# Kernel tuning notes

Measured on AMD Instinct MI355X. Metric: run time of the kernel, lower is better.

The kernel has to match this reference:

```python
import jax, jax.numpy as jnp
import numpy as np

HIDDEN = 512
HEADS = 8
HEAD_DIM = HIDDEN // HEADS
EPS_LN = 1e-5
EPS_ATTN = 1e-6


def setup_inputs() -> dict:
    key = jax.random.key(0)
    ks = jax.random.split(key, 12)
    B, S, N, D = 4, 12, 2048, HIDDEN
    s = 1.0 / np.sqrt(D)
    x = jax.random.normal(ks[0], (B, S, N, D), dtype=jnp.float32)
    Wq = jax.random.normal(ks[1], (D, D), dtype=jnp.float32) * s
    bq = jnp.zeros((D,), dtype=jnp.float32)
    Wk = jax.random.normal(ks[2], (D, D), dtype=jnp.float32) * s
    bk = jnp.zeros((D,), dtype=jnp.float32)
    Wv = jax.random.normal(ks[3], (D, D), dtype=jnp.float32) * s
    bv = jnp.zeros((D,), dtype=jnp.float32)
    Wo = jax.random.normal(ks[4], (D, D), dtype=jnp.float32) * s
    bo = jnp.zeros((D,), dtype=jnp.float32)
    ln_g = jnp.ones((D,), dtype=jnp.float32)
    ln_b = jnp.zeros((D,), dtype=jnp.float32)
    return {"x": x, "Wq": Wq, "bq": bq, "Wk": Wk, "bk": bk,
            "Wv": Wv, "bv": bv, "Wo": Wo, "bo": bo,
            "ln_g": ln_g, "ln_b": ln_b}


def _layer_norm(x, g, b):
    mu = jnp.mean(x, axis=-1, keepdims=True)
    var = jnp.var(x, axis=-1, keepdims=True)
    return (x - mu) * jax.lax.rsqrt(var + EPS_LN) * g + b


def reference(x, Wq, bq, Wk, bk, Wv, bv, Wo, bo, ln_g, ln_b):
    B, S, N, D = x.shape
    L = S * N  # flattened spatiotemporal tokens
    residual = x
    h = _layer_norm(x, ln_g, ln_b).reshape(B, L, D)
    # projections; [B, L, D] -> [B, H, L, hd]
    def split_heads(t):
        return t.reshape(B, L, HEADS, HEAD_DIM).transpose(0, 2, 1, 3)
    q = split_heads(h @ Wq.T + bq)
    k = split_heads(h @ Wk.T + bk)
    v = split_heads(h @ Wv.T + bv)
    # elu+1 feature map
    q = jax.nn.elu(q) + 1.0
    k = jax.nn.elu(k) + 1.0
    # kv outer product: [B, H, hd, hd]
    kv = jnp.einsum('bhld,bhle->bhde', k, v)
    out = jnp.einsum('bhld,bhde->bhle', q, kv)
    normalizer = jnp.einsum('bhld,bhd->bhl', q, k.sum(axis=2))
    out = out / (normalizer[..., None] + EPS_ATTN)
    out = out.transpose(0, 2, 1, 3).reshape(B, L, D)
    out = out @ Wo.T + bo
    out = out.reshape(B, S, N, D)
    return out + residual
```

## Files before the change

### kernel.cpp

```cpp
#include <hip/hip_runtime.h>
#include <hip/hip_bf16.h>
#include <stdint.h>

#define DDIM 512
#define NHEAD 8
#define BATCH 4
#define LTOK 24576
#define MROWS 98304
#define QKV_MBLK 384
#define KVCH 96
#define PTILE 4160

typedef __attribute__((ext_vector_type(8))) short short8;
typedef __attribute__((ext_vector_type(4))) float f32x4;

__device__ __forceinline__ float bf2f(unsigned short u) {
  union { unsigned int i; float f; } c; c.i = ((unsigned int)u) << 16; return c.f;
}
__device__ __forceinline__ unsigned short f2bf(float f) {
  __hip_bfloat16 h = __float2bfloat16(f);
  return __builtin_bit_cast(unsigned short, h);
}
__device__ __forceinline__ void gload16(const void* g, void* l) {
  __builtin_amdgcn_global_load_lds((const __attribute__((address_space(1))) void*)g,
                                   (__attribute__((address_space(3))) void*)l, 16, 0, 0);
}
__device__ __forceinline__ float elu1(float v) { return (v > 0.f) ? (v + 1.f) : __expf(v); }

__global__ __launch_bounds__(256) void wprep(const float* __restrict__ Wq, const float* __restrict__ bq,
                                             const float* __restrict__ Wk, const float* __restrict__ bk,
                                             const float* __restrict__ Wv, const float* __restrict__ bv,
                                             const float* __restrict__ Wo,
                                             unsigned short* __restrict__ wf,
                                             unsigned short* __restrict__ wob,
                                             float* __restrict__ biasf) {
  long t = (long)blockIdx.x * 256 + threadIdx.x;
  if (t < 786432) {
    int f = (int)(t >> 9), c = (int)(t & 511);
    const float* src;
    if (f < 1024) { int hh = f >> 7, kv = (f >> 6) & 1, d = f & 63;
                    src = (kv ? Wv : Wk) + (long)(hh * 64 + d) * 512; }
    else          src = Wq + (long)(f - 1024) * 512;
    wf[t] = f2bf(src[c]);
  } else if (t < 786432 + 262144) {
    long i = t - 786432; wob[i] = f2bf(Wo[i]);
  } else if (t < 786432 + 262144 + 1536) {
    int f = (int)(t - (786432 + 262144));
    float v;
    if (f < 1024) { int hh = f >> 7, kv = (f >> 6) & 1, d = f & 63; v = (kv ? bv : bk)[hh * 64 + d]; }
    else v = bq[f - 1024];
    biasf[f] = v;
  }
}

__global__ __launch_bounds__(256) void ln_kernel(const float* __restrict__ x,
                                                 const float* __restrict__ g,
                                                 const float* __restrict__ b,
                                                 unsigned short* __restrict__ h) {
  int wv = threadIdx.x >> 6, lane = threadIdx.x & 63;
  long row = (long)blockIdx.x * 4 + wv;
  const float* xr = x + row * DDIM + lane * 8;
  float4 v0 = *(const float4*)xr;
  float4 v1 = *(const float4*)(xr + 4);
  float s  = v0.x + v0.y + v0.z + v0.w + v1.x + v1.y + v1.z + v1.w;
  float s2 = v0.x*v0.x + v0.y*v0.y + v0.z*v0.z + v0.w*v0.w
           + v1.x*v1.x + v1.y*v1.y + v1.z*v1.z + v1.w*v1.w;
  #pragma unroll
  for (int o = 32; o; o >>= 1) { s += __shfl_xor(s, o); s2 += __shfl_xor(s2, o); }
  float mu = s * (1.0f / DDIM);
  float var = s2 * (1.0f / DDIM) - mu * mu;
  float rs = rsqrtf(var + 1e-5f);
  float4 g0 = *(const float4*)(g + lane * 8);
  float4 g1 = *(const float4*)(g + lane * 8 + 4);
  float4 b0 = *(const float4*)(b + lane * 8);
  float4 b1 = *(const float4*)(b + lane * 8 + 4);
  short8 o;
  o[0] = (short)f2bf((v0.x - mu) * rs * g0.x + b0.x);
  o[1] = (short)f2bf((v0.y - mu) * rs * g0.y + b0.y);
  o[2] = (short)f2bf((v0.z - mu) * rs * g0.z + b0.z);
  o[3] = (short)f2bf((v0.w - mu) * rs * g0.w + b0.w);
  o[4] = (short)f2bf((v1.x - mu) * rs * g1.x + b1.x);
  o[5] = (short)f2bf((v1.y - mu) * rs * g1.y + b1.y);
  o[6] = (short)f2bf((v1.z - mu) * rs * g1.z + b1.z);
  o[7] = (short)f2bf((v1.w - mu) * rs * g1.w + b1.w);
  *(short8*)(h + row * DDIM + lane * 8) = o;
}

__device__ __forceinline__ short8 ldsfrag(const unsigned short* h, int row, int kg) {
  return *(const short8*)&h[row * 32 + ((kg ^ ((row >> 1) & 3)) << 3)];
}

__device__ __forceinline__ void stage_half(const unsigned short* gbase,
                                           unsigned short* ldsbase, int tid) {
  #pragma unroll
  for (int i = 0; i < 2; i++) {
    int c = i * 512 + tid;
    int rr = c >> 2, cc = c & 3;
    int sc = ((cc ^ ((rr >> 1) & 3)) << 3);
    gload16(gbase + (long)rr * DDIM + sc, ldsbase + c * 8);
  }
}

template <int VMP1, int VMP3, bool S01, bool S23>
__device__ __forceinline__ void ktile(int t, unsigned short* lds,
                                      const unsigned short* Ab, const unsigned short* Wb,
                                      f32x4 (&acc)[8][4],
                                      int wm, int wn, int lr, int kg, int tid) {
  const int buf = t & 1;
  unsigned short* A0l = lds + (buf * 2 + 0) * 8192;
  unsigned short* A1l = lds + (buf * 2 + 1) * 8192;
  unsigned short* B0l = lds + 32768 + (buf * 2 + 0) * 8192;
  unsigned short* B1l = lds + 32768 + (buf * 2 + 1) * 8192;
  unsigned short* A1n = lds + ((buf ^ 1) * 2 + 1) * 8192;
  unsigned short* B1n = lds + 32768 + ((buf ^ 1) * 2 + 1) * 8192;
  short8 a[4], b[4];

  #pragma unroll
  for (int m = 0; m < 4; m++) a[m] = ldsfrag(A0l, wm * 128 + m * 16 + lr, kg);
  #pragma unroll
  for (int n = 0; n < 4; n++) b[n] = ldsfrag(B0l, wn * 64 + n * 16 + lr, kg);
  if (S01) stage_half(Ab + (long)(t + 1) * 64 + 32, A1n, tid);
  __builtin_amdgcn_s_barrier();
  __builtin_amdgcn_s_setprio(1);
  #pragma unroll
  for (int m = 0; m < 4; m++)
    #pragma unroll
    for (int n = 0; n < 4; n++)
      acc[m][n] = __builtin_amdgcn_mfma_f32_16x16x32_bf16(a[m], b[n], acc[m][n], 0, 0, 0);
  __builtin_amdgcn_s_setprio(0);
  __builtin_amdgcn_s_barrier();
  __builtin_amdgcn_sched_barrier(0);

  #pragma unroll
  for (int m = 0; m < 4; m++) a[m] = ldsfrag(A0l, wm * 128 + (4 + m) * 16 + lr, kg);
  if (S01) stage_half(Wb + (long)(t + 1) * 64 + 32, B1n, tid);
  __builtin_amdgcn_s_barrier();
  __builtin_amdgcn_s_setprio(1);
  #pragma unroll
  for (int m = 0; m < 4; m++)
    #pragma unroll
    for (int n = 0; n < 4; n++)
      acc[4 + m][n] = __builtin_amdgcn_mfma_f32_16x16x32_bf16(a[m], b[n], acc[4 + m][n], 0, 0, 0);
  __builtin_amdgcn_s_setprio(0);
  asm volatile("s_waitcnt vmcnt(%0)" :: "i"(VMP1) : "memory");
  __builtin_amdgcn_s_barrier();
  __builtin_amdgcn_sched_barrier(0);

  #pragma unroll
  for (int m = 0; m < 4; m++) a[m] = ldsfrag(A1l, wm * 128 + m * 16 + lr, kg);
  #pragma unroll
  for (int n = 0; n < 4; n++) b[n] = ldsfrag(B1l, wn * 64 + n * 16 + lr, kg);
  if (S23) stage_half(Ab + (long)(t + 2) * 64, A0l, tid);
  __builtin_amdgcn_s_barrier();
  __builtin_amdgcn_s_setprio(1);
  #pragma unroll
  for (int m = 0; m < 4; m++)
    #pragma unroll
    for (int n = 0; n < 4; n++)
      acc[m][n] = __builtin_amdgcn_mfma_f32_16x16x32_bf16(a[m], b[n], acc[m][n], 0, 0, 0);
  __builtin_amdgcn_s_setprio(0);
  __builtin_amdgcn_s_barrier();
  __builtin_amdgcn_sched_barrier(0);

  #pragma unroll
  for (int m = 0; m < 4; m++) a[m] = ldsfrag(A1l, wm * 128 + (4 + m) * 16 + lr, kg);
  if (S23) stage_half(Wb + (long)(t + 2) * 64, B0l, tid);
  __builtin_amdgcn_s_barrier();
  __builtin_amdgcn_s_setprio(1);
  #pragma unroll
  for (int m = 0; m < 4; m++)
    #pragma unroll
    for (int n = 0; n < 4; n++)
      acc[4 + m][n] = __builtin_amdgcn_mfma_f32_16x16x32_bf16(a[m], b[n], acc[4 + m][n], 0, 0, 0);
  __builtin_amdgcn_s_setprio(0);
  asm volatile("s_waitcnt vmcnt(%0)" :: "i"(VMP3) : "memory");
  __builtin_amdgcn_s_barrier();
  __builtin_amdgcn_sched_barrier(0);
}

__device__ __forceinline__ void kloop256(unsigned short* lds,
                                         const unsigned short* Ab, const unsigned short* Wb,
                                         f32x4 (&acc)[8][4],
                                         int wm, int wn, int lr, int kg, int tid) {
  stage_half(Ab,       lds + 0 * 8192, tid);
  stage_half(Wb,       lds + 32768 + 0 * 8192, tid);
  stage_half(Ab + 32,  lds + 1 * 8192, tid);
  stage_half(Wb + 32,  lds + 32768 + 1 * 8192, tid);
  stage_half(Ab + 64,  lds + 2 * 8192, tid);
  stage_half(Wb + 64,  lds + 32768 + 2 * 8192, tid);
  asm volatile("s_waitcnt vmcnt(8)" ::: "memory");
  __builtin_amdgcn_s_barrier();
  __builtin_amdgcn_sched_barrier(0);

  #pragma unroll 1
  for (int i = 0; i < 3; i++) {
    ktile<8, 8, true, true>(2 * i,     lds, Ab, Wb, acc, wm, wn, lr, kg, tid);
    ktile<8, 8, true, true>(2 * i + 1, lds, Ab, Wb, acc, wm, wn, lr, kg, tid);
  }
  ktile<8, 4, true, false>(6, lds, Ab, Wb, acc, wm, wn, lr, kg, tid);
  ktile<0, 63, false, false>(7, lds, Ab, Wb, acc, wm, wn, lr, kg, tid);
}

__global__ __launch_bounds__(512, 2) void qkv_gemm(const unsigned short* __restrict__ A,
                                                   const unsigned short* __restrict__ wf,
                                                   const float* __restrict__ biasf,
                                                   unsigned short* __restrict__ qbuf,
                                                   unsigned short* __restrict__ part) {
  __shared__ unsigned short lds[65536];

  int tid = threadIdx.x;
  int wv = tid >> 6, lane = tid & 63;
  int wm = wv >> 2, wn = wv & 3;
  int kg = lane >> 4, lr = lane & 15;

  int lin = blockIdx.x;
  int g = lin / 48, r = lin % 48;
  int xb = g * 8 + (r & 7);
  int y  = r >> 3;
  long mBase = (long)xb * 256;
  int nBase = y * 256;

  const unsigned short* Ab = A + mBase * DDIM;
  const unsigned short* Wb = wf + (long)nBase * DDIM;

  f32x4 acc[8][4];
  #pragma unroll
  for (int m = 0; m < 8; m++)
    #pragma unroll
    for (int n = 0; n < 4; n++) acc[m][n] = (f32x4){0.f, 0.f, 0.f, 0.f};

  kloop256(lds, Ab, Wb, acc, wm, wn, lr, kg, tid);
  __syncthreads();

  if (y < 4) {
    unsigned short* kT = lds;
    unsigned short* vT = lds + 16896;
    int batch = xb / KVCH;
    int cIdx  = xb % KVCH;

    {
      int rr = 64 + (tid >> 5), cc = tid & 31;
      short8 z;
      #pragma unroll
      for (int j = 0; j < 8; j++) z[j] = (rr == 64) ? (short)0x3F80 : (short)0;
      *(short8*)&vT[rr * 264 + cc * 8] = z;
    }

    #pragma unroll 1
    for (int p = 0; p < 2; p++) {
      if ((wn >> 1) == p) {
        bool isV = wn & 1;
        #pragma unroll
        for (int n = 0; n < 4; n++) {
          int feat = n * 16 + lr;
          float bv = biasf[nBase + wn * 64 + n * 16 + lr];
          #pragma unroll
          for (int m = 0; m < 8; m++)
            #pragma unroll
            for (int j = 0; j < 4; j++) {
              int tok = wm * 128 + m * 16 + kg * 4 + j;
              float v = acc[m][n][j] + bv;
              if (!isV) kT[feat * 264 + tok] = f2bf(elu1(v));
              else      vT[feat * 264 + tok] = f2bf(v);
            }
        }
      }
      __syncthreads();

      int mt = wv & 3, ngrp = wv >> 2;
      int h = y * 2 + p;
      long pbase = ((long)(batch * 8 + h) * KVCH + cIdx) * PTILE;
      if (!ngrp) {
        f32x4 pa0 = {0,0,0,0}, pa1 = {0,0,0,0}, pa2 = {0,0,0,0};
        #pragma unroll
        for (int kk = 0; kk < 8; kk++) {
          short8 af = *(const short8*)&kT[(mt * 16 + lr) * 264 + kk * 32 + kg * 8];
          short8 b0 = *(const short8*)&vT[(0 * 16 + lr) * 264 + kk * 32 + kg * 8];
          short8 b1 = *(const short8*)&vT[(1 * 16 + lr) * 264 + kk * 32 + kg * 8];
          short8 b2 = *(const short8*)&vT[(2 * 16 + lr) * 264 + kk * 32 + kg * 8];
          pa0 = __builtin_amdgcn_mfma_f32_16x16x32_bf16(af, b0, pa0, 0, 0, 0);
          pa1 = __builtin_amdgcn_mfma_f32_16x16x32_bf16(af, b1, pa1, 0, 0, 0);
          pa2 = __builtin_amdgcn_mfma_f32_16x16x32_bf16(af, b2, pa2, 0, 0, 0);
        }
        #pragma unroll
        for (int j = 0; j < 4; j++) {
          int d = mt * 16 + kg * 4 + j;
          part[pbase + d * 64 + (0 * 16 + lr)] = f2bf(pa0[j]);
          part[pbase + d * 64 + (1 * 16 + lr)] = f2bf(pa1[j]);
          part[pbase + d * 64 + (2 * 16 + lr)] = f2bf(pa2[j]);
        }
      } else {
        f32x4 pa0 = {0,0,0,0}, pa1 = {0,0,0,0};
        #pragma unroll
        for (int kk = 0; kk < 8; kk++) {
          short8 af = *(const short8*)&kT[(mt * 16 + lr) * 264 + kk * 32 + kg * 8];
          short8 b0 = *(const short8*)&vT[(3 * 16 + lr) * 264 + kk * 32 + kg * 8];
          short8 b1 = *(const short8*)&vT[(4 * 16 + lr) * 264 + kk * 32 + kg * 8];
          pa0 = __builtin_amdgcn_mfma_f32_16x16x32_bf16(af, b0, pa0, 0, 0, 0);
          pa1 = __builtin_amdgcn_mfma_f32_16x16x32_bf16(af, b1, pa1, 0, 0, 0);
        }
        #pragma unroll
        for (int j = 0; j < 4; j++) {
          int d = mt * 16 + kg * 4 + j;
          part[pbase + d * 64 + (3 * 16 + lr)] = f2bf(pa0[j]);
          if (lr == 0) part[pbase + 4096 + d] = f2bf(pa1[j]);
        }
      }
      __syncthreads();
    }
  } else {
    unsigned short* Cs = lds;
    int qc0 = (y - 4) * 256;
    #pragma unroll 1
    for (int half = 0; half < 2; half++) {
      if (wm == half) {
        #pragma unroll
        for (int n = 0; n < 4; n++) {
          int col = wn * 64 + n * 16 + lr;
          float bv = biasf[nBase + col];
          #pragma unroll
          for (int m = 0; m < 8; m++)
            #pragma unroll
            for (int j = 0; j < 4; j++) {
              int rowl = m * 16 + kg * 4 + j;
              Cs[rowl * 264 + col] = f2bf(elu1(acc[m][n][j] + bv));
            }
        }
      }
      __syncthreads();
      #pragma unroll
      for (int i = 0; i < 8; i++) {
        int idx = i * 512 + tid;
        int row = idx >> 5, ch = idx & 31;
        *(short8*)&qbuf[(mBase + half * 128 + row) * DDIM + qc0 + ch * 8] =
            *(const short8*)&Cs[row * 264 + ch * 8];
      }
      __syncthreads();
    }
  }
}

__global__ __launch_bounds__(256) void kv_final(const unsigned short* __restrict__ part,
                                                unsigned short* __restrict__ kvD,
                                                float* __restrict__ ksum) {
  int bh = blockIdx.x;
  int gidx = blockIdx.y * 256 + threadIdx.x;
  if (gidx >= 520) return;
  long idx0 = (long)gidx * 8;
  const unsigned short* base = part + (long)bh * KVCH * PTILE + idx0;
  float s[8];
  #pragma unroll
  for (int j = 0; j < 8; j++) s[j] = 0.f;
  #pragma unroll 4
  for (int c = 0; c < KVCH; c++) {
    short8 v = *(const short8*)(base + (long)c * PTILE);
    #pragma unroll
    for (int j = 0; j < 8; j++) s[j] += bf2f((unsigned short)v[j]);
  }
  if (idx0 < 4096) {
    short8 o;
    #pragma unroll
    for (int j = 0; j < 8; j++) o[j] = (short)f2bf(s[j]);
    *(short8*)&kvD[bh * 4096 + idx0] = o;
  } else {
    int d0 = (int)(idx0 - 4096);
    #pragma unroll
    for (int j = 0; j < 8; j++) ksum[bh * 64 + d0 + j] = s[j];
  }
}

__global__ __launch_bounds__(512) void w2_gemm(const unsigned short* __restrict__ kvD,
                                               const unsigned short* __restrict__ wob,
                                               unsigned short* __restrict__ Bmat) {
  __shared__ unsigned short W2s[512 * 72];
  int t = threadIdx.x, wv = t >> 6, lane = t & 63;
  int kg = lane >> 4, lr = lane & 15;
  int bh = blockIdx.x, b = bh >> 3, h = bh & 7;
  const unsigned short* kva = kvD + bh * 4096;

  short8 a[4][2];
  #pragma unroll
  for (int m = 0; m < 4; m++)
    #pragma unroll
    for (int kk = 0; kk < 2; kk++)
      a[m][kk] = *(const short8*)&kva[(m * 16 + lr) * 64 + kk * 32 + kg * 8];

  f32x4 acc[4][4];
  #pragma unroll
  for (int m = 0; m < 4; m++)
    #pragma unroll
    for (int n = 0; n < 4; n++) acc[m][n] = (f32x4){0.f, 0.f, 0.f, 0.f};

  #pragma unroll
  for (int n = 0; n < 4; n++) {
    int c = wv * 64 + n * 16 + lr;
    #pragma unroll
    for (int kk = 0; kk < 2; kk++) {
      short8 bfr = *(const short8*)&wob[(long)c * 512 + h * 64 + kk * 32 + kg * 8];
      #pragma unroll
      for (int m = 0; m < 4; m++)
        acc[m][n] = __builtin_amdgcn_mfma_f32_16x16x32_bf16(a[m][kk], bfr, acc[m][n], 0, 0, 0);
    }
  }
  #pragma unroll
  for (int m = 0; m < 4; m++)
    #pragma unroll
    for (int n = 0; n < 4; n++)
      #pragma unroll
      for (int j = 0; j < 4; j++)
        W2s[(wv * 64 + n * 16 + lr) * 72 + m * 16 + kg * 4 + j] = f2bf(acc[m][n][j]);
  __syncthreads();
  #pragma unroll
  for (int pp = 0; pp < 8; pp++) {
    int idx = pp * 512 + t;
    int c = idx >> 3, ch = (idx & 7) * 8;
    *(short8*)&Bmat[(long)b * 262144 + (long)c * 512 + h * 64 + ch] =
        *(const short8*)&W2s[c * 72 + ch];
  }
}

__global__ __launch_bounds__(256) void qscale(unsigned short* __restrict__ q,
                                              const float* __restrict__ ksum) {
  int wv = threadIdx.x >> 6, lane = threadIdx.x & 63;
  long row = (long)blockIdx.x * 4 + wv;
  int batch = (int)(row / LTOK);
  int bh = batch * 8 + (lane >> 3);
  unsigned short* qr = q + row * DDIM + lane * 8;
  short8 qv = *(const short8*)qr;
  const float* ks = ksum + bh * 64 + (lane & 7) * 8;
  float4 k0 = *(const float4*)ks;
  float4 k1 = *(const float4*)(ks + 4);
  float qf[8];
  #pragma unroll
  for (int j = 0; j < 8; j++) qf[j] = bf2f((unsigned short)qv[j]);
  float n = qf[0]*k0.x + qf[1]*k0.y + qf[2]*k0.z + qf[3]*k0.w
          + qf[4]*k1.x + qf[5]*k1.y + qf[6]*k1.z + qf[7]*k1.w;
  n += __shfl_xor(n, 1);
  n += __shfl_xor(n, 2);
  n += __shfl_xor(n, 4);
  float s = 1.0f / (n + 1e-6f);
  short8 o;
  #pragma unroll
  for (int j = 0; j < 8; j++) o[j] = (short)f2bf(qf[j] * s);
  *(short8*)qr = o;
}

__global__ __launch_bounds__(512, 2) void ogemm(const unsigned short* __restrict__ A,
                                                const unsigned short* __restrict__ Bm,
                                                const float* __restrict__ bo,
                                                const float* __restrict__ xres,
                                                float* __restrict__ out) {
  __shared__ unsigned short lds[65536];

  int tid = threadIdx.x;
  int wv = tid >> 6, lane = tid & 63;
  int wm = wv >> 2, wn = wv & 3;
  int kg = lane >> 4, lr = lane & 15;

  int lin = blockIdx.x;
  int g = lin >> 4, r = lin & 15;
  int xb = g * 8 + (r & 7);
  int y  = r >> 3;
  long mBase = (long)xb * 256;
  int nBase = y * 256;
  int batch = xb / 96;

  const unsigned short* Ab = A + mBase * DDIM;
  const unsigned short* Wb = Bm + (long)batch * 262144 + (long)nBase * DDIM;

  f32x4 acc[8][4];
  #pragma unroll
  for (int m = 0; m < 8; m++)
    #pragma unroll
    for (int n = 0; n < 4; n++) acc[m][n] = (f32x4){0.f, 0.f, 0.f, 0.f};

  kloop256(lds, Ab, Wb, acc, wm, wn, lr, kg, tid);
  __syncthreads();

  float* Cs = (float*)lds;
  #pragma unroll 1
  for (int half = 0; half < 2; half++) {
    if (wm == half) {
      #pragma unroll
      for (int n = 0; n < 4; n++) {
        int col = wn * 64 + n * 16 + lr;
        float bv = bo[nBase + col];
        #pragma unroll
        for (int m = 0; m < 8; m++)
          #pragma unroll
          for (int j = 0; j < 4; j++) {
            int lrow = m * 16 + kg * 4 + j;
            Cs[lrow * 256 + (col ^ (((lrow >> 2) & 3) << 4))] = acc[m][n][j] + bv;
          }
      }
    }
    __syncthreads();
    #pragma unroll
    for (int it = 0; it < 16; it++) {
      int idx = it * 512 + tid;
      int row = idx >> 6, c4 = idx & 63;
      int pcol = (c4 * 4) ^ (((row >> 2) & 3) << 4);
      long goff = (mBase + half * 128 + row) * DDIM + nBase + c4 * 4;
      float4 rv = *(const float4*)&xres[goff];
      float4 cv = *(const float4*)&Cs[row * 256 + pcol];
      float4 ov; ov.x = cv.x + rv.x; ov.y = cv.y + rv.y; ov.z = cv.z + rv.z; ov.w = cv.w + rv.w;
      *(float4*)&out[goff] = ov;
    }
    __syncthreads();
  }
}

extern "C" void kernel_launch(void* const* d_in, const int* in_sizes, int n_in,
                              void* d_out, int out_size, void* d_ws, size_t ws_size,
                              hipStream_t stream) {
  const float* x    = (const float*)d_in[0];
  const float* Wq   = (const float*)d_in[1];
  const float* bq   = (const float*)d_in[2];
  const float* Wk   = (const float*)d_in[3];
  const float* bk   = (const float*)d_in[4];
  const float* Wv   = (const float*)d_in[5];
  const float* bv   = (const float*)d_in[6];
  const float* Wo   = (const float*)d_in[7];
  const float* bo   = (const float*)d_in[8];
  const float* ln_g = (const float*)d_in[9];
  const float* ln_b = (const float*)d_in[10];

  char* ws = (char*)d_ws;
  size_t SZ = (size_t)MROWS * DDIM * 2;
  unsigned short* hbuf = (unsigned short*)ws;
  unsigned short* qbuf = (unsigned short*)(ws + SZ);
  char* p = ws + 2 * SZ;
  unsigned short* wf   = (unsigned short*)p;  p += (size_t)1536 * 512 * 2;
  unsigned short* wob  = (unsigned short*)p;  p += (size_t)512 * 512 * 2;
  float* biasf         = (float*)p;           p += 1536 * 4;
  p = (char*)(((uintptr_t)p + 255) & ~(uintptr_t)255);
  unsigned short* part = (unsigned short*)p;  p += (size_t)32 * KVCH * PTILE * 2;
  unsigned short* kvD  = (unsigned short*)p;  p += (size_t)32 * 4096 * 2;
  float* ksum          = (float*)p;           p += 32 * 64 * 4;
  p = (char*)(((uintptr_t)p + 255) & ~(uintptr_t)255);
  unsigned short* Bmat = (unsigned short*)p;  p += (size_t)BATCH * 512 * 512 * 2;

  wprep<<<(786432 + 262144 + 1536 + 255) / 256, 256, 0, stream>>>(Wq, bq, Wk, bk, Wv, bv, Wo,
                                                                  wf, wob, biasf);
  ln_kernel<<<MROWS / 4, 256, 0, stream>>>(x, ln_g, ln_b, hbuf);
  qkv_gemm<<<QKV_MBLK * 6, 512, 0, stream>>>(hbuf, wf, biasf, qbuf, part);
  kv_final<<<dim3(32, 3), 256, 0, stream>>>(part, kvD, ksum);
  w2_gemm<<<32, 512, 0, stream>>>(kvD, wob, Bmat);
  qscale<<<MROWS / 4, 256, 0, stream>>>(qbuf, ksum);
  ogemm<<<QKV_MBLK * 2, 512, 0, stream>>>(qbuf, Bmat, bo, x, (float*)d_out);
}
```

Baseline: 492.8 us.

## Shrink GEMM tiles to 256x128 with triple-buffered K loop for higher occupancy

```diff
diff --git a/kernel.cpp b/kernel.cpp
--- a/kernel.cpp
+++ b/kernel.cpp
@@ -7,7 +7,7 @@
 #define BATCH 4
 #define LTOK 24576
 #define MROWS 98304
-#define QKV_MBLK 384
+#define MPNL 384
 #define KVCH 96
 #define PTILE 4160
 
@@ -86,153 +86,99 @@
   *(short8*)(h + row * DDIM + lane * 8) = o;
 }
 
+
 __device__ __forceinline__ short8 ldsfrag(const unsigned short* h, int row, int kg) {
   return *(const short8*)&h[row * 32 + ((kg ^ ((row >> 1) & 3)) << 3)];
 }
 
-__device__ __forceinline__ void stage_half(const unsigned short* gbase,
-                                           unsigned short* ldsbase, int tid) {
+__device__ __forceinline__ void stageA(const unsigned short* g, unsigned short* l, int tid) {
   #pragma unroll
   for (int i = 0; i < 2; i++) {
     int c = i * 512 + tid;
     int rr = c >> 2, cc = c & 3;
     int sc = ((cc ^ ((rr >> 1) & 3)) << 3);
-    gload16(gbase + (long)rr * DDIM + sc, ldsbase + c * 8);
-  }
-}
-
-template <int VMP1, int VMP3, bool S01, bool S23>
-__device__ __forceinline__ void ktile(int t, unsigned short* lds,
+    gload16(g + (long)rr * DDIM + sc, l + c * 8);
+  }
+}
+__device__ __forceinline__ void stageB(const unsigned short* g, unsigned short* l, int tid) {
+  int c = tid;
+  int rr = c >> 2, cc = c & 3;
+  int sc = ((cc ^ ((rr >> 1) & 3)) << 3);
+  gload16(g + (long)rr * DDIM + sc, l + c * 8);
+}
+
+__device__ __forceinline__ void kloop(unsigned short* lds,
                                       const unsigned short* Ab, const unsigned short* Wb,
-                                      f32x4 (&acc)[8][4],
+                                      f32x4 (&acc)[4][4],
                                       int wm, int wn, int lr, int kg, int tid) {
-  const int buf = t & 1;
-  unsigned short* A0l = lds + (buf * 2 + 0) * 8192;
-  unsigned short* A1l = lds + (buf * 2 + 1) * 8192;
-  unsigned short* B0l = lds + 32768 + (buf * 2 + 0) * 8192;
-  unsigned short* B1l = lds + 32768 + (buf * 2 + 1) * 8192;
-  unsigned short* A1n = lds + ((buf ^ 1) * 2 + 1) * 8192;
-  unsigned short* B1n = lds + 32768 + ((buf ^ 1) * 2 + 1) * 8192;
-  short8 a[4], b[4];
-
-  #pragma unroll
-  for (int m = 0; m < 4; m++) a[m] = ldsfrag(A0l, wm * 128 + m * 16 + lr, kg);
-  #pragma unroll
-  for (int n = 0; n < 4; n++) b[n] = ldsfrag(B0l, wn * 64 + n * 16 + lr, kg);
-  if (S01) stage_half(Ab + (long)(t + 1) * 64 + 32, A1n, tid);
-  __builtin_amdgcn_s_barrier();
-  __builtin_amdgcn_s_setprio(1);
-  #pragma unroll
-  for (int m = 0; m < 4; m++)
-    #pragma unroll
-    for (int n = 0; n < 4; n++)
-      acc[m][n] = __builtin_amdgcn_mfma_f32_16x16x32_bf16(a[m], b[n], acc[m][n], 0, 0, 0);
-  __builtin_amdgcn_s_setprio(0);
+  stageA(Ab,      lds + 0 * 8192, tid);  stageB(Wb,      lds + 24576 + 0 * 4096, tid);
+  stageA(Ab + 32, lds + 1 * 8192, tid);  stageB(Wb + 32, lds + 24576 + 1 * 4096, tid);
+  asm volatile("s_waitcnt vmcnt(3)" ::: "memory");
   __builtin_amdgcn_s_barrier();
   __builtin_amdgcn_sched_barrier(0);
 
-  #pragma unroll
-  for (int m = 0; m < 4; m++) a[m] = ldsfrag(A0l, wm * 128 + (4 + m) * 16 + lr, kg);
-  if (S01) stage_half(Wb + (long)(t + 1) * 64 + 32, B1n, tid);
-  __builtin_amdgcn_s_barrier();
-  __builtin_amdgcn_s_setprio(1);
-  #pragma unroll
-  for (int m = 0; m < 4; m++)
-    #pragma unroll
-    for (int n = 0; n < 4; n++)
-      acc[4 + m][n] = __builtin_amdgcn_mfma_f32_16x16x32_bf16(a[m], b[n], acc[4 + m][n], 0, 0, 0);
-  __builtin_amdgcn_s_setprio(0);
-  asm volatile("s_waitcnt vmcnt(%0)" :: "i"(VMP1) : "memory");
-  __builtin_amdgcn_s_barrier();
-  __builtin_amdgcn_sched_barrier(0);
-
-  #pragma unroll
-  for (int m = 0; m < 4; m++) a[m] = ldsfrag(A1l, wm * 128 + m * 16 + lr, kg);
-  #pragma unroll
-  for (int n = 0; n < 4; n++) b[n] = ldsfrag(B1l, wn * 64 + n * 16 + lr, kg);
-  if (S23) stage_half(Ab + (long)(t + 2) * 64, A0l, tid);
-  __builtin_amdgcn_s_barrier();
-  __builtin_amdgcn_s_setprio(1);
-  #pragma unroll
-  for (int m = 0; m < 4; m++)
-    #pragma unroll
-    for (int n = 0; n < 4; n++)
-      acc[m][n] = __builtin_amdgcn_mfma_f32_16x16x32_bf16(a[m], b[n], acc[m][n], 0, 0, 0);
-  __builtin_amdgcn_s_setprio(0);
-  __builtin_amdgcn_s_barrier();
-  __builtin_amdgcn_sched_barrier(0);
-
-  #pragma unroll
-  for (int m = 0; m < 4; m++) a[m] = ldsfrag(A1l, wm * 128 + (4 + m) * 16 + lr, kg);
-  if (S23) stage_half(Wb + (long)(t + 2) * 64, B0l, tid);
-  __builtin_amdgcn_s_barrier();
-  __builtin_amdgcn_s_setprio(1);
-  #pragma unroll
-  for (int m = 0; m < 4; m++)
-    #pragma unroll
-    for (int n = 0; n < 4; n++)
-      acc[4 + m][n] = __builtin_amdgcn_mfma_f32_16x16x32_bf16(a[m], b[n], acc[4 + m][n], 0, 0, 0);
-  __builtin_amdgcn_s_setprio(0);
-  asm volatile("s_waitcnt vmcnt(%0)" :: "i"(VMP3) : "memory");
-  __builtin_amdgcn_s_barrier();
-  __builtin_amdgcn_sched_barrier(0);
-}
-
-__device__ __forceinline__ void kloop256(unsigned short* lds,
-                                         const unsigned short* Ab, const unsigned short* Wb,
-                                         f32x4 (&acc)[8][4],
-                                         int wm, int wn, int lr, int kg, int tid) {
-  stage_half(Ab,       lds + 0 * 8192, tid);
-  stage_half(Wb,       lds + 32768 + 0 * 8192, tid);
-  stage_half(Ab + 32,  lds + 1 * 8192, tid);
-  stage_half(Wb + 32,  lds + 32768 + 1 * 8192, tid);
-  stage_half(Ab + 64,  lds + 2 * 8192, tid);
-  stage_half(Wb + 64,  lds + 32768 + 2 * 8192, tid);
-  asm volatile("s_waitcnt vmcnt(8)" ::: "memory");
-  __builtin_amdgcn_s_barrier();
-  __builtin_amdgcn_sched_barrier(0);
-
   #pragma unroll 1
-  for (int i = 0; i < 3; i++) {
-    ktile<8, 8, true, true>(2 * i,     lds, Ab, Wb, acc, wm, wn, lr, kg, tid);
-    ktile<8, 8, true, true>(2 * i + 1, lds, Ab, Wb, acc, wm, wn, lr, kg, tid);
-  }
-  ktile<8, 4, true, false>(6, lds, Ab, Wb, acc, wm, wn, lr, kg, tid);
-  ktile<0, 63, false, false>(7, lds, Ab, Wb, acc, wm, wn, lr, kg, tid);
-}
-
-__global__ __launch_bounds__(512, 2) void qkv_gemm(const unsigned short* __restrict__ A,
+  for (int t = 0; t < 16; ++t) {
+    const unsigned short* As = lds + (t % 3) * 8192;
+    const unsigned short* Bs = lds + 24576 + (t % 3) * 4096;
+    short8 a[4], b[4];
+    #pragma unroll
+    for (int m = 0; m < 4; m++) a[m] = ldsfrag(As, wm * 64 + m * 16 + lr, kg);
+    #pragma unroll
+    for (int n = 0; n < 4; n++) b[n] = ldsfrag(Bs, wn * 64 + n * 16 + lr, kg);
+    if (t < 14) {
+      int s = (t + 2) % 3;
+      stageA(Ab + (long)(t + 2) * 32, lds + s * 8192, tid);
+      stageB(Wb + (long)(t + 2) * 32, lds + 24576 + s * 4096, tid);
+    }
+    __builtin_amdgcn_s_setprio(1);
+    #pragma unroll
+    for (int m = 0; m < 4; m++)
+      #pragma unroll
+      for (int n = 0; n < 4; n++)
+        acc[m][n] = __builtin_amdgcn_mfma_f32_16x16x32_bf16(a[m], b[n], acc[m][n], 0, 0, 0);
+    __builtin_amdgcn_s_setprio(0);
+    if (t < 14)       { asm volatile("s_waitcnt vmcnt(3)" ::: "memory"); }
+    else if (t == 14) { asm volatile("s_waitcnt vmcnt(0)" ::: "memory"); }
+    if (t < 15) {
+      __builtin_amdgcn_s_barrier();
+      __builtin_amdgcn_sched_barrier(0);
+    }
+  }
+}
+
+__global__ __launch_bounds__(512, 4) void qkv_gemm(const unsigned short* __restrict__ A,
                                                    const unsigned short* __restrict__ wf,
                                                    const float* __restrict__ biasf,
                                                    unsigned short* __restrict__ qbuf,
                                                    unsigned short* __restrict__ part) {
-  __shared__ unsigned short lds[65536];
+  __shared__ unsigned short lds[38016];
 
   int tid = threadIdx.x;
   int wv = tid >> 6, lane = tid & 63;
-  int wm = wv >> 2, wn = wv & 3;
+  int wm = wv >> 1, wn = wv & 1;
   int kg = lane >> 4, lr = lane & 15;
 
   int lin = blockIdx.x;
-  int g = lin / 48, r = lin % 48;
+  int g = lin / 96, r = lin % 96;
   int xb = g * 8 + (r & 7);
   int y  = r >> 3;
   long mBase = (long)xb * 256;
-  int nBase = y * 256;
+  int nBase = y * 128;
 
   const unsigned short* Ab = A + mBase * DDIM;
   const unsigned short* Wb = wf + (long)nBase * DDIM;
 
-  f32x4 acc[8][4];
-  #pragma unroll
-  for (int m = 0; m < 8; m++)
+  f32x4 acc[4][4];
+  #pragma unroll
+  for (int m = 0; m < 4; m++)
     #pragma unroll
     for (int n = 0; n < 4; n++) acc[m][n] = (f32x4){0.f, 0.f, 0.f, 0.f};
 
-  kloop256(lds, Ab, Wb, acc, wm, wn, lr, kg, tid);
+  kloop(lds, Ab, Wb, acc, wm, wn, lr, kg, tid);
   __syncthreads();
 
-  if (y < 4) {
+  if (y < 8) {
     unsigned short* kT = lds;
     unsigned short* vT = lds + 16896;
     int batch = xb / KVCH;
@@ -246,96 +192,82 @@
       *(short8*)&vT[rr * 264 + cc * 8] = z;
     }
 
-    #pragma unroll 1
-    for (int p = 0; p < 2; p++) {
-      if ((wn >> 1) == p) {
-        bool isV = wn & 1;
-        #pragma unroll
-        for (int n = 0; n < 4; n++) {
-          int feat = n * 16 + lr;
-          float bv = biasf[nBase + wn * 64 + n * 16 + lr];
-          #pragma unroll
-          for (int m = 0; m < 8; m++)
-            #pragma unroll
-            for (int j = 0; j < 4; j++) {
-              int tok = wm * 128 + m * 16 + kg * 4 + j;
-              float v = acc[m][n][j] + bv;
-              if (!isV) kT[feat * 264 + tok] = f2bf(elu1(v));
-              else      vT[feat * 264 + tok] = f2bf(v);
-            }
-        }
-      }
-      __syncthreads();
-
-      int mt = wv & 3, ngrp = wv >> 2;
-      int h = y * 2 + p;
-      long pbase = ((long)(batch * 8 + h) * KVCH + cIdx) * PTILE;
-      if (!ngrp) {
-        f32x4 pa0 = {0,0,0,0}, pa1 = {0,0,0,0}, pa2 = {0,0,0,0};
-        #pragma unroll
-        for (int kk = 0; kk < 8; kk++) {
-          short8 af = *(const short8*)&kT[(mt * 16 + lr) * 264 + kk * 32 + kg * 8];
-          short8 b0 = *(const short8*)&vT[(0 * 16 + lr) * 264 + kk * 32 + kg * 8];
-          short8 b1 = *(const short8*)&vT[(1 * 16 + lr) * 264 + kk * 32 + kg * 8];
-          short8 b2 = *(const short8*)&vT[(2 * 16 + lr) * 264 + kk * 32 + kg * 8];
-          pa0 = __builtin_amdgcn_mfma_f32_16x16x32_bf16(af, b0, pa0, 0, 0, 0);
-          pa1 = __builtin_amdgcn_mfma_f32_16x16x32_bf16(af, b1, pa1, 0, 0, 0);
-          pa2 = __builtin_amdgcn_mfma_f32_16x16x32_bf16(af, b2, pa2, 0, 0, 0);
-        }
+    #pragma unroll
+    for (int n = 0; n < 4; n++) {
+      int feat = n * 16 + lr;
+      float bv = biasf[nBase + wn * 64 + feat];
+      #pragma unroll
+      for (int m = 0; m < 4; m++)
         #pragma unroll
         for (int j = 0; j < 4; j++) {
-          int d = mt * 16 + kg * 4 + j;
-          part[pbase + d * 64 + (0 * 16 + lr)] = f2bf(pa0[j]);
-          part[pbase + d * 64 + (1 * 16 + lr)] = f2bf(pa1[j]);
-          part[pbase + d * 64 + (2 * 16 + lr)] = f2bf(pa2[j]);
+          int tok = wm * 64 + m * 16 + kg * 4 + j;
+          float v = acc[m][n][j] + bv;
+          if (wn == 0) kT[feat * 264 + tok] = f2bf(elu1(v));
+          else         vT[feat * 264 + tok] = f2bf(v);
         }
-      } else {
-        f32x4 pa0 = {0,0,0,0}, pa1 = {0,0,0,0};
-        #pragma unroll
-        for (int kk = 0; kk < 8; kk++) {
-          short8 af = *(const short8*)&kT[(mt * 16 + lr) * 264 + kk * 32 + kg * 8];
-          short8 b0 = *(const short8*)&vT[(3 * 16 + lr) * 264 + kk * 32 + kg * 8];
-          short8 b1 = *(const short8*)&vT[(4 * 16 + lr) * 264 + kk * 32 + kg * 8];
-          pa0 = __builtin_amdgcn_mfma_f32_16x16x32_bf16(af, b0, pa0, 0, 0, 0);
-          pa1 = __builtin_amdgcn_mfma_f32_16x16x32_bf16(af, b1, pa1, 0, 0, 0);
-        }
+    }
+    __syncthreads();
+
+    int mt = wv & 3, ngrp = wv >> 2;
+    long pbase = ((long)(batch * 8 + y) * KVCH + cIdx) * PTILE;
+    if (!ngrp) {
+      f32x4 pa0 = {0,0,0,0}, pa1 = {0,0,0,0}, pa2 = {0,0,0,0};
+      #pragma unroll
+      for (int kk = 0; kk < 8; kk++) {
+        short8 af = *(const short8*)&kT[(mt * 16 + lr) * 264 + kk * 32 + kg * 8];
+        short8 b0 = *(const short8*)&vT[(0 * 16 + lr) * 264 + kk * 32 + kg * 8];
+        short8 b1 = *(const short8*)&vT[(1 * 16 + lr) * 264 + kk * 32 + kg * 8];
+        short8 b2 = *(const short8*)&vT[(2 * 16 + lr) * 264 + kk * 32 + kg * 8];
+        pa0 = __builtin_amdgcn_mfma_f32_16x16x32_bf16(af, b0, pa0, 0, 0, 0);
+        pa1 = __builtin_amdgcn_mfma_f32_16x16x32_bf16(af, b1, pa1, 0, 0, 0);
+        pa2 = __builtin_amdgcn_mfma_f32_16x16x32_bf16(af, b2, pa2, 0, 0, 0);
+      }
+      #pragma unroll
+      for (int j = 0; j < 4; j++) {
+        int d = mt * 16 + kg * 4 + j;
+        part[pbase + d * 64 + (0 * 16 + lr)] = f2bf(pa0[j]);
+        part[pbase + d * 64 + (1 * 16 + lr)] = f2bf(pa1[j]);
+        part[pbase + d * 64 + (2 * 16 + lr)] = f2bf(pa2[j]);
+      }
+    } else {
+      f32x4 pa0 = {0,0,0,0}, pa1 = {0,0,0,0};
+      #pragma unroll
+      for (int kk = 0; kk < 8; kk++) {
+        short8 af = *(const short8*)&kT[(mt * 16 + lr) * 264 + kk * 32 + kg * 8];
+        short8 b0 = *(const short8*)&vT[(3 * 16 + lr) * 264 + kk * 32 + kg * 8];
+        short8 b1 = *(const short8*)&vT[(4 * 16 + lr) * 264 + kk * 32 + kg * 8];
+        pa0 = __builtin_amdgcn_mfma_f32_16x16x32_bf16(af, b0, pa0, 0, 0, 0);
+        pa1 = __builtin_amdgcn_mfma_f32_16x16x32_bf16(af, b1, pa1, 0, 0, 0);
+      }
+      #pragma unroll
+      for (int j = 0; j < 4; j++) {
+        int d = mt * 16 + kg * 4 + j;
+        part[pbase + d * 64 + (3 * 16 + lr)] = f2bf(pa0[j]);
+        if (lr == 0) part[pbase + 4096 + d] = f2bf(pa1[j]);
+      }
+    }
+  } else {
+    unsigned short* Cs = lds;
+    int qc0 = (y - 8) * 128;
+    #pragma unroll
+    for (int n = 0; n < 4; n++) {
+      int col = wn * 64 + n * 16 + lr;
+      float bv = biasf[nBase + col];
+      #pragma unroll
+      for (int m = 0; m < 4; m++)
         #pragma unroll
         for (int j = 0; j < 4; j++) {
-          int d = mt * 16 + kg * 4 + j;
-          part[pbase + d * 64 + (3 * 16 + lr)] = f2bf(pa0[j]);
-          if (lr == 0) part[pbase + 4096 + d] = f2bf(pa1[j]);
+          int row = wm * 64 + m * 16 + kg * 4 + j;
+          Cs[row * 136 + col] = f2bf(elu1(acc[m][n][j] + bv));
         }
-      }
-      __syncthreads();
-    }
-  } else {
-    unsigned short* Cs = lds;
-    int qc0 = (y - 4) * 256;
-    #pragma unroll 1
-    for (int half = 0; half < 2; half++) {
-      if (wm == half) {
-        #pragma unroll
-        for (int n = 0; n < 4; n++) {
-          int col = wn * 64 + n * 16 + lr;
-          float bv = biasf[nBase + col];
-          #pragma unroll
-          for (int m = 0; m < 8; m++)
-            #pragma unroll
-            for (int j = 0; j < 4; j++) {
-              int rowl = m * 16 + kg * 4 + j;
-              Cs[rowl * 264 + col] = f2bf(elu1(acc[m][n][j] + bv));
-            }
-        }
-      }
-      __syncthreads();
-      #pragma unroll
-      for (int i = 0; i < 8; i++) {
-        int idx = i * 512 + tid;
-        int row = idx >> 5, ch = idx & 31;
-        *(short8*)&qbuf[(mBase + half * 128 + row) * DDIM + qc0 + ch * 8] =
-            *(const short8*)&Cs[row * 264 + ch * 8];
-      }
-      __syncthreads();
+    }
+    __syncthreads();
+    #pragma unroll
+    for (int i = 0; i < 8; i++) {
+      int idx = i * 512 + tid;
+      int row = idx >> 4, ch = idx & 15;
+      *(short8*)&qbuf[(mBase + row) * DDIM + qc0 + ch * 8] =
+          *(const short8*)&Cs[row * 136 + ch * 8];
     }
   }
 }
@@ -445,64 +377,63 @@
   *(short8*)qr = o;
 }
 
-__global__ __launch_bounds__(512, 2) void ogemm(const unsigned short* __restrict__ A,
+__global__ __launch_bounds__(512, 4) void ogemm(const unsigned short* __restrict__ A,
                                                 const unsigned short* __restrict__ Bm,
                                                 const float* __restrict__ bo,
                                                 const float* __restrict__ xres,
                                                 float* __restrict__ out) {
-  __shared__ unsigned short lds[65536];
+  __shared__ unsigned short lds[38016];
 
   int tid = threadIdx.x;
   int wv = tid >> 6, lane = tid & 63;
-  int wm = wv >> 2, wn = wv & 3;
+  int wm = wv >> 1, wn = wv & 1;
   int kg = lane >> 4, lr = lane & 15;
 
   int lin = blockIdx.x;
-  int g = lin >> 4, r = lin & 15;
+  int g = lin >> 5, r = lin & 31;
   int xb = g * 8 + (r & 7);
   int y  = r >> 3;
   long mBase = (long)xb * 256;
-  int nBase = y * 256;
-  int batch = xb / 96;
+  int nBase = y * 128;
+  int batch = xb / KVCH;
 
   const unsigned short* Ab = A + mBase * DDIM;
   const unsigned short* Wb = Bm + (long)batch * 262144 + (long)nBase * DDIM;
 
-  f32x4 acc[8][4];
-  #pragma unroll
-  for (int m = 0; m < 8; m++)
+  f32x4 acc[4][4];
+  #pragma unroll
+  for (int m = 0; m < 4; m++)
     #pragma unroll
     for (int n = 0; n < 4; n++) acc[m][n] = (f32x4){0.f, 0.f, 0.f, 0.f};
 
-  kloop256(lds, Ab, Wb, acc, wm, wn, lr, kg, tid);
+  kloop(lds, Ab, Wb, acc, wm, wn, lr, kg, tid);
   __syncthreads();
 
   float* Cs = (float*)lds;
   #pragma unroll 1
-  for (int half = 0; half < 2; half++) {
-    if (wm == half) {
+  for (int rr = 0; rr < 2; rr++) {
+    if ((wm >> 1) == rr) {
       #pragma unroll
       for (int n = 0; n < 4; n++) {
         int col = wn * 64 + n * 16 + lr;
         float bv = bo[nBase + col];
         #pragma unroll
-        for (int m = 0; m < 8; m++)
+        for (int m = 0; m < 4; m++)
           #pragma unroll
           for (int j = 0; j < 4; j++) {
-            int lrow = m * 16 + kg * 4 + j;
-            Cs[lrow * 256 + (col ^ (((lrow >> 2) & 3) << 4))] = acc[m][n][j] + bv;
+            int lrow = (wm & 1) * 64 + m * 16 + kg * 4 + j;
+            Cs[lrow * 132 + col] = acc[m][n][j] + bv;
           }
       }
     }
     __syncthreads();
     #pragma unroll
-    for (int it = 0; it < 16; it++) {
+    for (int it = 0; it < 8; it++) {
       int idx = it * 512 + tid;
-      int row = idx >> 6, c4 = idx & 63;
-      int pcol = (c4 * 4) ^ (((row >> 2) & 3) << 4);
-      long goff = (mBase + half * 128 + row) * DDIM + nBase + c4 * 4;
+      int row = idx >> 5, c4 = idx & 31;
+      long goff = (mBase + rr * 128 + row) * DDIM + nBase + c4 * 4;
       float4 rv = *(const float4*)&xres[goff];
-      float4 cv = *(const float4*)&Cs[row * 256 + pcol];
+      float4 cv = *(const float4*)&Cs[row * 132 + c4 * 4];
       float4 ov; ov.x = cv.x + rv.x; ov.y = cv.y + rv.y; ov.z = cv.z + rv.z; ov.w = cv.w + rv.w;
       *(float4*)&out[goff] = ov;
     }
@@ -543,9 +474,9 @@
   wprep<<<(786432 + 262144 + 1536 + 255) / 256, 256, 0, stream>>>(Wq, bq, Wk, bk, Wv, bv, Wo,
                                                                   wf, wob, biasf);
   ln_kernel<<<MROWS / 4, 256, 0, stream>>>(x, ln_g, ln_b, hbuf);
-  qkv_gemm<<<QKV_MBLK * 6, 512, 0, stream>>>(hbuf, wf, biasf, qbuf, part);
+  qkv_gemm<<<MPNL * 12, 512, 0, stream>>>(hbuf, wf, biasf, qbuf, part);
   kv_final<<<dim3(32, 3), 256, 0, stream>>>(part, kvD, ksum);
   w2_gemm<<<32, 512, 0, stream>>>(kvD, wob, Bmat);
   qscale<<<MROWS / 4, 256, 0, stream>>>(qbuf, ksum);
-  ogemm<<<QKV_MBLK * 2, 512, 0, stream>>>(qbuf, Bmat, bo, x, (float*)d_out);
-}
+  ogemm<<<MPNL * 4, 512, 0, stream>>>(qbuf, Bmat, bo, x, (float*)d_out);
+}
```

Measured after the change: 420.1 us. -14.8%, faster.
